# Kernel optimization log

Hardware: AMD Instinct MI355X
Metric: run time of the kernel (lower is better)

Reference implementation:

```python
import jax, jax.numpy as jnp
import numpy as np

SLOPE = 25.0   # snntorch surrogate.fast_sigmoid default slope
THR = 1.0      # snntorch Leaky default threshold
NUM_STEPS = 100

# fast_sigmoid surrogate spike: heaviside fwd, 1/(slope|x|+1)^2 bwd
@jax.custom_vjp
def spike(x):
    return (x > 0).astype(x.dtype)

def _spike_fwd(x):
    return spike(x), x

def _spike_bwd(x, g):
    return (g / (SLOPE * jnp.abs(x) + 1.0) ** 2,)

spike.defvjp(_spike_fwd, _spike_bwd)


def setup_inputs() -> dict:
    key = jax.random.key(0)
    ks = jax.random.split(key, 5)
    B, D_in, D_h, D_out = 512, 784, 2048, 10
    x = jax.random.normal(ks[0], (B, D_in), dtype=jnp.float32)
    W1 = jax.random.normal(ks[1], (D_h, D_in), dtype=jnp.float32) / np.sqrt(D_in).astype(np.float32)
    b1 = jax.random.normal(ks[2], (D_h,), dtype=jnp.float32) * 0.01
    W2 = jax.random.normal(ks[3], (D_out, D_h), dtype=jnp.float32) / np.sqrt(D_h).astype(np.float32)
    b2 = jax.random.normal(ks[4], (D_out,), dtype=jnp.float32) * 0.01
    beta1 = jnp.asarray(0.9, dtype=jnp.float32)  # learn_beta=True -> parameter
    beta2 = jnp.asarray(0.9, dtype=jnp.float32)
    return {"x": x, "W1": W1, "b1": b1, "W2": W2, "b2": b2, "beta1": beta1, "beta2": beta2}


def reference(x, W1, b1, W2, b2, beta1, beta2):
    dtype = x.dtype
    B = x.shape[0]
    Dh = W1.shape[0]
    Do = W2.shape[0]
    # fc1(x) is loop-invariant in the original (x constant across steps) -> hoist
    cur1 = x @ W1.T + b1                       # [B, Dh]
    b1c = jnp.clip(beta1, 0.0, 1.0)            # snntorch clamps beta in forward
    b2c = jnp.clip(beta2, 0.0, 1.0)
    mem1_0 = jnp.zeros((B, Dh), dtype)         # init_leaky -> 0
    mem2_0 = jnp.zeros((B, Do), dtype)

    def step(carry, _):
        mem1, mem2 = carry
        # snntorch Leaky (reset_mechanism='subtract'):
        # reset_t = detached heaviside(mem_{t-1} - thr); mem_t = beta*mem_{t-1} + cur - reset*thr
        reset1 = jax.lax.stop_gradient((mem1 > THR).astype(dtype))
        mem1 = b1c * mem1 + cur1 - reset1 * THR
        spk1 = spike(mem1 - THR)               # [B, Dh]
        cur2 = spk1 @ W2.T + b2                # [B, Do]
        reset2 = jax.lax.stop_gradient((mem2 > THR).astype(dtype))
        mem2 = b2c * mem2 + cur2 - reset2 * THR
        spk2 = spike(mem2 - THR)
        return (mem1, mem2), spk2

    _, spk2_rec = jax.lax.scan(step, (mem1_0, mem2_0), None, length=NUM_STEPS)  # [T, B, Do]
    # snn_res_step_num == snn_num_steps -> mean over all steps
    stk_mean = jnp.mean(spk2_rec, axis=0)      # [B, Do]
    return jax.nn.softmax(stk_mean, axis=1)
```

## Files before the change

### kernel.cpp

```cpp
#include <hip/hip_runtime.h>
#include <cstdint>

typedef unsigned int u32;
typedef unsigned short u16;
typedef unsigned long long u64;
typedef __attribute__((ext_vector_type(4))) float f32x4;
typedef __attribute__((ext_vector_type(8))) short s16x8;

#define D_IN   784
#define D_H    2048
#define D_O    10
#define T_STEPS 100

static __device__ __forceinline__ u16 f2bf_rn(float f) {
  u32 u = __float_as_uint(f);
  u32 r = u + 0x7FFFu + ((u >> 16) & 1u);
  return (u16)(r >> 16);
}
static __device__ __forceinline__ float bf2f(u16 h) {
  return __uint_as_float(((u32)h) << 16);
}

static __device__ __forceinline__ void packpair(float f0, float f1,
                                                u32& o0, u32& o1, u32& o2) {
  u32 u0 = __float_as_uint(f0), u1 = __float_as_uint(f1);
  o0 = (u0 >> 16) | (u1 & 0xFFFF0000u);
  float r0 = __fsub_rn(f0, __uint_as_float(u0 & 0xFFFF0000u));
  float r1 = __fsub_rn(f1, __uint_as_float(u1 & 0xFFFF0000u));
  u32 v0 = __float_as_uint(r0), v1 = __float_as_uint(r1);
  o1 = (v0 >> 16) | (v1 & 0xFFFF0000u);
  float s0 = __fsub_rn(r0, __uint_as_float(v0 & 0xFFFF0000u));
  float s1 = __fsub_rn(r1, __uint_as_float(v1 & 0xFFFF0000u));
  o2 = (__float_as_uint(s0) >> 16) | (__float_as_uint(s1) & 0xFFFF0000u);
}

__global__ __launch_bounds__(256) void k_prep_w2(const float* __restrict__ W2,
                                                 u32* __restrict__ Phi,
                                                 u32* __restrict__ Plo) {
  int t = blockIdx.x * 256 + threadIdx.x;
  if (t >= 64 * 64) return;
  int kb = t >> 6, l = t & 63;
  int o = l & 15;
  int kbase = kb * 32 + ((l >> 4) << 3);
  u32 hw[4], lw[4];
#pragma unroll
  for (int p = 0; p < 4; ++p) {
    u32 hp = 0, lp = 0;
#pragma unroll
    for (int q = 0; q < 2; ++q) {
      float f = (o < D_O) ? W2[o * D_H + kbase + 2 * p + q] : 0.0f;
      u16 h = f2bf_rn(f);
      float rr = __fsub_rn(f, bf2f(h));
      u16 lo = f2bf_rn(rr);
      hp |= ((u32)h) << (16 * q);
      lp |= ((u32)lo) << (16 * q);
    }
    hw[p] = hp; lw[p] = lp;
  }
  int base = (kb * 64 + l) * 4;
#pragma unroll
  for (int p = 0; p < 4; ++p) { Phi[base + p] = hw[p]; Plo[base + p] = lw[p]; }
}

__global__ __launch_bounds__(512) void k_fgemm(const float* __restrict__ x,
                                               const float* __restrict__ W1,
                                               const float* __restrict__ b1,
                                               float* __restrict__ cur1) {
  __shared__ uint4 As[3][4][64];
  __shared__ uint4 Bs[3][4][64];
  const int tid = threadIdx.x, wave = tid >> 6, lane = tid & 63;
  const int id = blockIdx.x;
  const int sub = id >> 3;
  const int mb = sub >> 2;
  const int nb = (id & 7) * 4 + (sub & 3);
  const int wm = wave >> 1, wn = wave & 1;
  const int st = tid & 255;
  const int srow = st >> 2, skq = st & 3;
  const int sfrag = srow >> 4;
  const int slane = skq * 16 + (srow & 15);
  const bool isA = (tid < 256);
  const float* srcrow = isA ? (x  + (size_t)(mb * 64 + srow) * D_IN)
                            : (W1 + (size_t)(nb * 64 + srow) * D_IN);
  f32x4 acc0 = {0.f, 0.f, 0.f, 0.f}, acc1 = {0.f, 0.f, 0.f, 0.f};
  float e[8];
  {
    const int kg = skq * 8;
    float4 v0 = *(const float4*)(srcrow + kg);
    float4 v1 = *(const float4*)(srcrow + kg + 4);
    e[0] = v0.x; e[1] = v0.y; e[2] = v0.z; e[3] = v0.w;
    e[4] = v1.x; e[5] = v1.y; e[6] = v1.z; e[7] = v1.w;
  }
  for (int kb = 0; kb < 25; ++kb) {
    u32 w0[4], w1[4], w2[4];
#pragma unroll
    for (int p = 0; p < 4; ++p) packpair(e[2 * p], e[2 * p + 1], w0[p], w1[p], w2[p]);
    __syncthreads();
    if (isA) {
      As[0][sfrag][slane] = make_uint4(w0[0], w0[1], w0[2], w0[3]);
      As[1][sfrag][slane] = make_uint4(w1[0], w1[1], w1[2], w1[3]);
      As[2][sfrag][slane] = make_uint4(w2[0], w2[1], w2[2], w2[3]);
    } else {
      Bs[0][sfrag][slane] = make_uint4(w0[0], w0[1], w0[2], w0[3]);
      Bs[1][sfrag][slane] = make_uint4(w1[0], w1[1], w1[2], w1[3]);
      Bs[2][sfrag][slane] = make_uint4(w2[0], w2[1], w2[2], w2[3]);
    }
    __syncthreads();
    if (kb < 24) {
      const int kg = (kb + 1) * 32 + skq * 8;
      if (kg < D_IN) {
        float4 v0 = *(const float4*)(srcrow + kg);
        float4 v1 = *(const float4*)(srcrow + kg + 4);
        e[0] = v0.x; e[1] = v0.y; e[2] = v0.z; e[3] = v0.w;
        e[4] = v1.x; e[5] = v1.y; e[6] = v1.z; e[7] = v1.w;
      } else {
#pragma unroll
        for (int q = 0; q < 8; ++q) e[q] = 0.0f;
      }
    }
    s16x8 A0 = __builtin_bit_cast(s16x8, As[0][wm][lane]);
    s16x8 A1 = __builtin_bit_cast(s16x8, As[1][wm][lane]);
    s16x8 A2 = __builtin_bit_cast(s16x8, As[2][wm][lane]);
    {
      s16x8 B0 = __builtin_bit_cast(s16x8, Bs[0][wn * 2][lane]);
      s16x8 B1 = __builtin_bit_cast(s16x8, Bs[1][wn * 2][lane]);
      s16x8 B2 = __builtin_bit_cast(s16x8, Bs[2][wn * 2][lane]);
      acc0 = __builtin_amdgcn_mfma_f32_16x16x32_bf16(A0, B0, acc0, 0, 0, 0);
      acc0 = __builtin_amdgcn_mfma_f32_16x16x32_bf16(A0, B1, acc0, 0, 0, 0);
      acc0 = __builtin_amdgcn_mfma_f32_16x16x32_bf16(A1, B0, acc0, 0, 0, 0);
      acc0 = __builtin_amdgcn_mfma_f32_16x16x32_bf16(A1, B1, acc0, 0, 0, 0);
      acc0 = __builtin_amdgcn_mfma_f32_16x16x32_bf16(A0, B2, acc0, 0, 0, 0);
      acc0 = __builtin_amdgcn_mfma_f32_16x16x32_bf16(A2, B0, acc0, 0, 0, 0);
    }
    {
      s16x8 B0 = __builtin_bit_cast(s16x8, Bs[0][wn * 2 + 1][lane]);
      s16x8 B1 = __builtin_bit_cast(s16x8, Bs[1][wn * 2 + 1][lane]);
      s16x8 B2 = __builtin_bit_cast(s16x8, Bs[2][wn * 2 + 1][lane]);
      acc1 = __builtin_amdgcn_mfma_f32_16x16x32_bf16(A0, B0, acc1, 0, 0, 0);
      acc1 = __builtin_amdgcn_mfma_f32_16x16x32_bf16(A0, B1, acc1, 0, 0, 0);
      acc1 = __builtin_amdgcn_mfma_f32_16x16x32_bf16(A1, B0, acc1, 0, 0, 0);
      acc1 = __builtin_amdgcn_mfma_f32_16x16x32_bf16(A1, B1, acc1, 0, 0, 0);
      acc1 = __builtin_amdgcn_mfma_f32_16x16x32_bf16(A0, B2, acc1, 0, 0, 0);
      acc1 = __builtin_amdgcn_mfma_f32_16x16x32_bf16(A2, B0, acc1, 0, 0, 0);
    }
  }
  const int col = lane & 15, rb = (lane >> 4) * 4;
  {
    const int gcol = nb * 64 + (wn * 2) * 16 + col;
    const float bv = b1[gcol];
#pragma unroll
    for (int r = 0; r < 4; ++r)
      cur1[(size_t)(mb * 64 + wm * 16 + rb + r) * D_H + gcol] = acc0[r] + bv;
  }
  {
    const int gcol = nb * 64 + (wn * 2 + 1) * 16 + col;
    const float bv = b1[gcol];
#pragma unroll
    for (int r = 0; r < 4; ++r)
      cur1[(size_t)(mb * 64 + wm * 16 + rb + r) * D_H + gcol] = acc1[r] + bv;
  }
}

__global__ __launch_bounds__(512) void k_snn2(const float* __restrict__ cur1,
                                              const u32* __restrict__ Phi,
                                              const u32* __restrict__ Plo,
                                              const float* __restrict__ b2,
                                              const float* __restrict__ beta1p,
                                              const float* __restrict__ beta2p,
                                              float* __restrict__ out) {
  __shared__ u32  bitsS[64][112];
  __shared__ uint4 PhiS[8][64];
  __shared__ uint4 PloS[8][64];
  __shared__ float c2[112][18];
  const int b = blockIdx.x, tid = threadIdx.x;
  const int wave = tid >> 6, lane = tid & 63;
  const float b1c = fminf(fmaxf(beta1p[0], 0.0f), 1.0f);
  const float b2c = fminf(fmaxf(beta2p[0], 0.0f), 1.0f);

  float cv[4], memv[4]; bool sp[4];
  u32 alo[4], ahi[4];
#pragma unroll
  for (int j = 0; j < 4; ++j) {
    cv[j] = cur1[(size_t)b * D_H + j * 512 + tid];
    memv[j] = 0.0f; sp[j] = false; alo[j] = 0u; ahi[j] = 0u;
  }
  for (int t = 0; t < 64; ++t) {
    const bool mine = (lane == t);
#pragma unroll
    for (int j = 0; j < 4; ++j) {
      float m = __fmul_rn(b1c, memv[j]);
      m = __fadd_rn(m, cv[j]);
      if (sp[j]) m = __fsub_rn(m, 1.0f);
      sp[j] = (m > 1.0f);
      memv[j] = m;
      u64 msk = __ballot(sp[j]);
      alo[j] = mine ? (u32)msk : alo[j];
      ahi[j] = mine ? (u32)(msk >> 32) : ahi[j];
    }
  }
#pragma unroll
  for (int j = 0; j < 4; ++j) {
    bitsS[j * 16 + wave * 2 + 0][lane] = alo[j];
    bitsS[j * 16 + wave * 2 + 1][lane] = ahi[j];
    alo[j] = 0u; ahi[j] = 0u;
  }
  for (int t = 64; t < T_STEPS; ++t) {
    const bool mine = (lane == t - 64);
#pragma unroll
    for (int j = 0; j < 4; ++j) {
      float m = __fmul_rn(b1c, memv[j]);
      m = __fadd_rn(m, cv[j]);
      if (sp[j]) m = __fsub_rn(m, 1.0f);
      sp[j] = (m > 1.0f);
      memv[j] = m;
      u64 msk = __ballot(sp[j]);
      alo[j] = mine ? (u32)msk : alo[j];
      ahi[j] = mine ? (u32)(msk >> 32) : ahi[j];
    }
  }
  if (lane < 48) {
#pragma unroll
    for (int j = 0; j < 4; ++j) {
      bitsS[j * 16 + wave * 2 + 0][64 + lane] = alo[j];
      bitsS[j * 16 + wave * 2 + 1][64 + lane] = ahi[j];
    }
  }
  __syncthreads();

  f32x4 acc = {0.f, 0.f, 0.f, 0.f};
  const int trow = wave * 16 + (lane & 15);
  const int shift = (lane >> 4) * 8;
  for (int c = 0; c < 8; ++c) {
    PhiS[wave][lane] = *(const uint4*)(Phi + (size_t)((c * 8 + wave) * 64 + lane) * 4);
    PloS[wave][lane] = *(const uint4*)(Plo + (size_t)((c * 8 + wave) * 64 + lane) * 4);
    __syncthreads();
    if (wave < 7) {
#pragma unroll
      for (int kk = 0; kk < 8; ++kk) {
        u32 w8 = (bitsS[c * 8 + kk][trow] >> shift) & 0xFFu;
        u32 u = w8 | (w8 << 15);
        uint4 a0u;
        ((u32*)&a0u)[0] = ( u        & 0x00010001u) * 0x3F80u;
        ((u32*)&a0u)[1] = ((u >> 2)  & 0x00010001u) * 0x3F80u;
        ((u32*)&a0u)[2] = ((u >> 4)  & 0x00010001u) * 0x3F80u;
        ((u32*)&a0u)[3] = ((u >> 6)  & 0x00010001u) * 0x3F80u;
        s16x8 a   = __builtin_bit_cast(s16x8, a0u);
        s16x8 bhi = __builtin_bit_cast(s16x8, PhiS[kk][lane]);
        s16x8 blo = __builtin_bit_cast(s16x8, PloS[kk][lane]);
        acc = __builtin_amdgcn_mfma_f32_16x16x32_bf16(a, bhi, acc, 0, 0, 0);
        acc = __builtin_amdgcn_mfma_f32_16x16x32_bf16(a, blo, acc, 0, 0, 0);
      }
    }
    __syncthreads();
  }
  if (wave < 7) {
    const int colw = lane & 15, rbase = (lane >> 4) * 4;
#pragma unroll
    for (int r = 0; r < 4; ++r) c2[wave * 16 + rbase + r][colw] = acc[r];
  }
  __syncthreads();

  if (tid < 16) {
    const int o = tid;
    const bool valid = (o < D_O);
    const float bb = valid ? b2[o] : 0.0f;
    float m2 = 0.0f; bool s2 = false; int cnt = 0;
    for (int t0 = 0; t0 < T_STEPS; t0 += 10) {
      float cc[10];
#pragma unroll
      for (int i = 0; i < 10; ++i) cc[i] = c2[t0 + i][o];
#pragma unroll
      for (int i = 0; i < 10; ++i) {
        float cI = __fadd_rn(cc[i], bb);
        float m = __fadd_rn(__fmul_rn(b2c, m2), cI);
        if (s2) m = __fsub_rn(m, 1.0f);
        s2 = (m > 1.0f);
        m2 = m;
        cnt += s2 ? 1 : 0;
      }
    }
    float mean = valid ? ((float)cnt / 100.0f) : -1e30f;
    float mx = mean;
#pragma unroll
    for (int i = 8; i >= 1; i >>= 1) mx = fmaxf(mx, __shfl_xor(mx, i, 16));
    float e = valid ? expf(mean - mx) : 0.0f;
    float s = e;
#pragma unroll
    for (int i = 8; i >= 1; i >>= 1) s = __fadd_rn(s, __shfl_xor(s, i, 16));
    if (valid) out[(size_t)b * D_O + o] = e / s;
  }
}

extern "C" void kernel_launch(void* const* d_in, const int* in_sizes, int n_in,
                              void* d_out, int out_size, void* d_ws, size_t ws_size,
                              hipStream_t stream) {
  const float* x     = (const float*)d_in[0];
  const float* W1    = (const float*)d_in[1];
  const float* b1    = (const float*)d_in[2];
  const float* W2    = (const float*)d_in[3];
  const float* b2    = (const float*)d_in[4];
  const float* beta1 = (const float*)d_in[5];
  const float* beta2 = (const float*)d_in[6];
  float* out = (float*)d_out;

  char* ws = (char*)d_ws;
  float* cur1 = (float*)ws;
  u32*   Phi  = (u32*)(ws + 4194304);
  u32*   Plo  = (u32*)(ws + 4259840);

  hipLaunchKernelGGL(k_prep_w2, dim3(16), dim3(256), 0, stream, W2, Phi, Plo);
  hipLaunchKernelGGL(k_fgemm, dim3(256), dim3(512), 0, stream, x, W1, b1, cur1);
  hipLaunchKernelGGL(k_snn2, dim3(512), dim3(512), 0, stream,
                     cur1, Phi, Plo, b2, beta1, beta2, out);
}
```

Before: 73.98 us.

## Store spike ballots time-major in LDS and stream W2 fragments directly from global

```diff
diff --git a/kernel.cpp b/kernel.cpp
--- a/kernel.cpp
+++ b/kernel.cpp
@@ -160,99 +160,71 @@
   }
 }
 
-__global__ __launch_bounds__(512) void k_snn2(const float* __restrict__ cur1,
+__global__ __launch_bounds__(512) void k_snn3(const float* __restrict__ cur1,
                                               const u32* __restrict__ Phi,
                                               const u32* __restrict__ Plo,
                                               const float* __restrict__ b2,
                                               const float* __restrict__ beta1p,
                                               const float* __restrict__ beta2p,
                                               float* __restrict__ out) {
-  __shared__ u32  bitsS[64][112];
-  __shared__ uint4 PhiS[8][64];
-  __shared__ uint4 PloS[8][64];
+  __shared__ __align__(16) u32 bits[112][66];
   __shared__ float c2[112][18];
-  const int b = blockIdx.x, tid = threadIdx.x;
+  const int b = blockIdx.x;
+  const int tid = threadIdx.x;
   const int wave = tid >> 6, lane = tid & 63;
   const float b1c = fminf(fmaxf(beta1p[0], 0.0f), 1.0f);
   const float b2c = fminf(fmaxf(beta2p[0], 0.0f), 1.0f);
 
-  float cv[4], memv[4]; bool sp[4];
-  u32 alo[4], ahi[4];
+  for (int idx = tid; idx < 12 * 66; idx += 512) bits[100 + idx / 66][idx % 66] = 0;
+
+  float cv[4], memv[4], spf[4];
 #pragma unroll
   for (int j = 0; j < 4; ++j) {
     cv[j] = cur1[(size_t)b * D_H + j * 512 + tid];
-    memv[j] = 0.0f; sp[j] = false; alo[j] = 0u; ahi[j] = 0u;
-  }
-  for (int t = 0; t < 64; ++t) {
-    const bool mine = (lane == t);
+    memv[j] = 0.0f; spf[j] = 0.0f;
+  }
+  for (int t = 0; t < T_STEPS; ++t) {
+    u64 msk[4];
 #pragma unroll
     for (int j = 0; j < 4; ++j) {
       float m = __fmul_rn(b1c, memv[j]);
       m = __fadd_rn(m, cv[j]);
-      if (sp[j]) m = __fsub_rn(m, 1.0f);
-      sp[j] = (m > 1.0f);
+      m = __fsub_rn(m, spf[j]);
+      bool sp = (m > 1.0f);
+      msk[j] = __ballot(sp);
+      spf[j] = sp ? 1.0f : 0.0f;
       memv[j] = m;
-      u64 msk = __ballot(sp[j]);
-      alo[j] = mine ? (u32)msk : alo[j];
-      ahi[j] = mine ? (u32)(msk >> 32) : ahi[j];
-    }
-  }
-#pragma unroll
-  for (int j = 0; j < 4; ++j) {
-    bitsS[j * 16 + wave * 2 + 0][lane] = alo[j];
-    bitsS[j * 16 + wave * 2 + 1][lane] = ahi[j];
-    alo[j] = 0u; ahi[j] = 0u;
-  }
-  for (int t = 64; t < T_STEPS; ++t) {
-    const bool mine = (lane == t - 64);
-#pragma unroll
-    for (int j = 0; j < 4; ++j) {
-      float m = __fmul_rn(b1c, memv[j]);
-      m = __fadd_rn(m, cv[j]);
-      if (sp[j]) m = __fsub_rn(m, 1.0f);
-      sp[j] = (m > 1.0f);
-      memv[j] = m;
-      u64 msk = __ballot(sp[j]);
-      alo[j] = mine ? (u32)msk : alo[j];
-      ahi[j] = mine ? (u32)(msk >> 32) : ahi[j];
-    }
-  }
-  if (lane < 48) {
-#pragma unroll
-    for (int j = 0; j < 4; ++j) {
-      bitsS[j * 16 + wave * 2 + 0][64 + lane] = alo[j];
-      bitsS[j * 16 + wave * 2 + 1][64 + lane] = ahi[j];
+    }
+    if (lane == 0) {
+      u64* rowp = (u64*)&bits[t][0];
+      rowp[0 * 8 + wave] = msk[0];
+      rowp[1 * 8 + wave] = msk[1];
+      rowp[2 * 8 + wave] = msk[2];
+      rowp[3 * 8 + wave] = msk[3];
     }
   }
   __syncthreads();
 
-  f32x4 acc = {0.f, 0.f, 0.f, 0.f};
-  const int trow = wave * 16 + (lane & 15);
-  const int shift = (lane >> 4) * 8;
-  for (int c = 0; c < 8; ++c) {
-    PhiS[wave][lane] = *(const uint4*)(Phi + (size_t)((c * 8 + wave) * 64 + lane) * 4);
-    PloS[wave][lane] = *(const uint4*)(Plo + (size_t)((c * 8 + wave) * 64 + lane) * 4);
-    __syncthreads();
-    if (wave < 7) {
-#pragma unroll
-      for (int kk = 0; kk < 8; ++kk) {
-        u32 w8 = (bitsS[c * 8 + kk][trow] >> shift) & 0xFFu;
-        u32 u = w8 | (w8 << 15);
-        uint4 a0u;
-        ((u32*)&a0u)[0] = ( u        & 0x00010001u) * 0x3F80u;
-        ((u32*)&a0u)[1] = ((u >> 2)  & 0x00010001u) * 0x3F80u;
-        ((u32*)&a0u)[2] = ((u >> 4)  & 0x00010001u) * 0x3F80u;
-        ((u32*)&a0u)[3] = ((u >> 6)  & 0x00010001u) * 0x3F80u;
-        s16x8 a   = __builtin_bit_cast(s16x8, a0u);
-        s16x8 bhi = __builtin_bit_cast(s16x8, PhiS[kk][lane]);
-        s16x8 blo = __builtin_bit_cast(s16x8, PloS[kk][lane]);
-        acc = __builtin_amdgcn_mfma_f32_16x16x32_bf16(a, bhi, acc, 0, 0, 0);
-        acc = __builtin_amdgcn_mfma_f32_16x16x32_bf16(a, blo, acc, 0, 0, 0);
-      }
-    }
-    __syncthreads();
-  }
   if (wave < 7) {
+    f32x4 acc = {0.f, 0.f, 0.f, 0.f};
+    const int row0 = wave * 16 + (lane & 15);
+    const int shift = (lane >> 4) * 8;
+    for (int kb = 0; kb < 64; ++kb) {
+      const uint4 bh = *(const uint4*)(Phi + (size_t)(kb * 64 + lane) * 4);
+      const uint4 bl = *(const uint4*)(Plo + (size_t)(kb * 64 + lane) * 4);
+      u32 w8 = (bits[row0][kb] >> shift) & 0xFFu;
+      u32 u = w8 | (w8 << 15);
+      uint4 a0u;
+      ((u32*)&a0u)[0] = ( u        & 0x00010001u) * 0x3F80u;
+      ((u32*)&a0u)[1] = ((u >> 2)  & 0x00010001u) * 0x3F80u;
+      ((u32*)&a0u)[2] = ((u >> 4)  & 0x00010001u) * 0x3F80u;
+      ((u32*)&a0u)[3] = ((u >> 6)  & 0x00010001u) * 0x3F80u;
+      s16x8 a   = __builtin_bit_cast(s16x8, a0u);
+      s16x8 bhi = __builtin_bit_cast(s16x8, bh);
+      s16x8 blo = __builtin_bit_cast(s16x8, bl);
+      acc = __builtin_amdgcn_mfma_f32_16x16x32_bf16(a, bhi, acc, 0, 0, 0);
+      acc = __builtin_amdgcn_mfma_f32_16x16x32_bf16(a, blo, acc, 0, 0, 0);
+    }
     const int colw = lane & 15, rbase = (lane >> 4) * 4;
 #pragma unroll
     for (int r = 0; r < 4; ++r) c2[wave * 16 + rbase + r][colw] = acc[r];
@@ -309,6 +281,6 @@
 
   hipLaunchKernelGGL(k_prep_w2, dim3(16), dim3(256), 0, stream, W2, Phi, Plo);
   hipLaunchKernelGGL(k_fgemm, dim3(256), dim3(512), 0, stream, x, W1, b1, cur1);
-  hipLaunchKernelGGL(k_snn2, dim3(512), dim3(512), 0, stream,
+  hipLaunchKernelGGL(k_snn3, dim3(512), dim3(512), 0, stream,
                      cur1, Phi, Plo, b2, beta1, beta2, out);
 }
```

Result: faster. 69.87 us (-5.6%).
